# Optimization experiments

Measured on AMD Instinct MI355X. Metric: run time of the kernel, lower is better.

Reference implementation:

```python
import jax, jax.numpy as jnp
import numpy as np
import math

B, S, D = 2, 2048, 1024
H, KV, HD = 16, 4, 64
N_REP = H // KV
ROPE_THETA = 1.0e6


def _rope_tables(seq_len, head_dim, theta):
    inv_freq = 1.0 / (theta ** (np.arange(0, head_dim, 2, dtype=np.float32) / head_dim))
    t = np.arange(seq_len, dtype=np.float32)
    freqs = np.outer(t, inv_freq)                      # [S, HD/2]
    emb = np.concatenate([freqs, freqs], axis=-1)      # [S, HD]
    return jnp.asarray(np.cos(emb)), jnp.asarray(np.sin(emb))


def setup_inputs() -> dict:
    key = jax.random.key(0)
    ks = jax.random.split(key, 6)
    cos, sin = _rope_tables(S, HD, ROPE_THETA)
    scale = 0.02
    return {
        "x": jax.random.normal(ks[0], (B, S, D), dtype=jnp.float32),
        "cos": cos,
        "sin": sin,
        "Wq": jax.random.normal(ks[1], (D, H * HD), dtype=jnp.float32) * scale,
        "Wk": jax.random.normal(ks[2], (D, KV * HD), dtype=jnp.float32) * scale,
        "Wv": jax.random.normal(ks[3], (D, KV * HD), dtype=jnp.float32) * scale,
        "Wo": jax.random.normal(ks[4], (H * HD, D), dtype=jnp.float32) * scale,
    }


def _rotate_half(u):
    u1, u2 = u[..., : HD // 2], u[..., HD // 2 :]
    return jnp.concatenate([-u2, u1], axis=-1)


def reference(x, cos, sin, Wq, Wk, Wv, Wo):
    bsz, seq_len, _ = x.shape
    q = (x @ Wq).reshape(bsz, seq_len, H, HD)   # [B,S,H,HD]
    k = (x @ Wk).reshape(bsz, seq_len, KV, HD)  # [B,S,KV,HD]
    v = (x @ Wv).reshape(bsz, seq_len, KV, HD)

    # RoPE: cos/sin [S,HD] broadcast over batch and heads (unsqueeze_dim=1)
    c = cos[:seq_len][None, :, None, :]
    s = sin[:seq_len][None, :, None, :]
    q = q * c + _rotate_half(q) * s
    k = k * c + _rotate_half(k) * s

    # repeat_kv: expand KV heads groupwise to H heads
    k = jnp.repeat(k, N_REP, axis=2)  # [B,S,H,HD]
    v = jnp.repeat(v, N_REP, axis=2)

    q = q.transpose(0, 2, 1, 3)  # [B,H,S,HD]
    k = k.transpose(0, 2, 1, 3)
    v = v.transpose(0, 2, 1, 3)

    scores = jnp.einsum("bhqd,bhkd->bhqk", q, k) / math.sqrt(HD)
    causal = jnp.tril(jnp.ones((seq_len, seq_len), dtype=bool))
    scores = jnp.where(causal[None, None], scores, jnp.finfo(jnp.float32).min)
    probs = jax.nn.softmax(scores.astype(jnp.float32), axis=-1).astype(x.dtype)

    out = jnp.einsum("bhqk,bhkd->bhqd", probs, v)        # [B,H,S,HD]
    out = out.transpose(0, 2, 1, 3).reshape(bsz, seq_len, H * HD)
    return out @ Wo
```

## Files before the change

kernel.cpp:

```cpp
#include <hip/hip_runtime.h>

#define SS 2048
#define NH 16
#define NKV 4
#define HD 64

typedef __bf16 bf16;
typedef __bf16 bf16x8 __attribute__((ext_vector_type(8)));
typedef float f32x4 __attribute__((ext_vector_type(4)));

#define SM_SCALE 0.18033688011f

__device__ __forceinline__ void gl_lds16(const bf16* g, bf16* l) {
    __builtin_amdgcn_global_load_lds((const __attribute__((address_space(1))) void*)g,
                                     (__attribute__((address_space(3))) void*)l, 16, 0, 0);
}

__global__ __launch_bounds__(256) void prep_kernel(
    const float* __restrict__ x, const float* __restrict__ Wq, const float* __restrict__ Wk,
    const float* __restrict__ Wv, const float* __restrict__ Wo,
    bf16* __restrict__ xb, bf16* __restrict__ wqkv_t, bf16* __restrict__ wo_t)
{
    const int blk = blockIdx.x;
    const int tid = threadIdx.x;
    if (blk >= 640) {
        const float4* xv = (const float4*)x;
        const size_t base = (size_t)(blk - 640) * 2048 + tid;
        #pragma unroll
        for (int j = 0; j < 8; ++j) {
            const float4 v = xv[base + j * 256];
            bf16* o = xb + (base + j * 256) * 4;
            o[0] = (bf16)v.x; o[1] = (bf16)v.y; o[2] = (bf16)v.z; o[3] = (bf16)v.w;
        }
        return;
    }
    const float* W; bf16* Wt; int N, n0, k0;
    if (blk < 256)      { W = Wq; Wt = wqkv_t;                       N = 1024; n0 = (blk & 15) * 64;         k0 = (blk >> 4) * 64; }
    else if (blk < 320) { W = Wk; Wt = wqkv_t + (size_t)1024 * 1024; N = 256;  n0 = ((blk - 256) & 3) * 64;  k0 = ((blk - 256) >> 2) * 64; }
    else if (blk < 384) { W = Wv; Wt = wqkv_t + (size_t)1280 * 1024; N = 256;  n0 = ((blk - 320) & 3) * 64;  k0 = ((blk - 320) >> 2) * 64; }
    else                { W = Wo; Wt = wo_t;                         N = 1024; n0 = ((blk - 384) & 15) * 64; k0 = ((blk - 384) >> 4) * 64; }

    __shared__ float Ts[64][65];
    const int c = tid & 63, rr = tid >> 6;
    #pragma unroll
    for (int i = 0; i < 16; ++i) {
        const int kk = i * 4 + rr;
        Ts[kk][c] = W[(size_t)(k0 + kk) * N + n0 + c];
    }
    __syncthreads();
    #pragma unroll
    for (int i = 0; i < 16; ++i) {
        const int nn = i * 4 + rr;
        Wt[(size_t)(n0 + nn) * 1024 + k0 + c] = (bf16)Ts[c][nn];
    }
}

template<int EPI>
__global__ __launch_bounds__(256) void gemm_bt_kernel(
    const bf16* __restrict__ A, const bf16* __restrict__ Bt, float* __restrict__ C,
    const float* __restrict__ cosp, const float* __restrict__ sinp,
    bf16* __restrict__ qo, bf16* __restrict__ ko, bf16* __restrict__ vto,
    int M, int N, int K)
{
    __shared__ bf16 As[64 * 32];
    __shared__ bf16 Bs[128 * 32];
    const int m0 = blockIdx.x * 64, n0 = blockIdx.y * 128;
    const int tid = threadIdx.x;
    const int w = tid >> 6, lane = tid & 63, g = lane >> 4, li = lane & 15;
    const int wm = w >> 1, wn = w & 1;

    f32x4 acc[2][4];
    const f32x4 z = {0.f, 0.f, 0.f, 0.f};
    #pragma unroll
    for (int i = 0; i < 2; ++i)
        #pragma unroll
        for (int j = 0; j < 4; ++j) acc[i][j] = z;

    const int srow = tid >> 2, schunk = (tid & 3) * 8;
    const bf16* pA  = A  + (size_t)(m0 + srow) * K + schunk;
    const bf16* pB0 = Bt + (size_t)(n0 + srow) * K + schunk;
    const bf16* pB1 = Bt + (size_t)(n0 + 64 + srow) * K + schunk;
    bf16* lA  = As + (size_t)w * 512;
    bf16* lB0 = Bs + (size_t)w * 512;
    bf16* lB1 = Bs + 2048 + (size_t)w * 512;

    for (int kk = 0; kk < K; kk += 32) {
        __syncthreads();
        gl_lds16(pA + kk, lA);
        gl_lds16(pB0 + kk, lB0);
        gl_lds16(pB1 + kk, lB1);
        __syncthreads();
        bf16x8 af[2], bfr[4];
        #pragma unroll
        for (int mi = 0; mi < 2; ++mi) af[mi] = *(const bf16x8*)&As[(wm * 32 + mi * 16 + li) * 32 + g * 8];
        #pragma unroll
        for (int ni = 0; ni < 4; ++ni) bfr[ni] = *(const bf16x8*)&Bs[(wn * 64 + ni * 16 + li) * 32 + g * 8];
        #pragma unroll
        for (int mi = 0; mi < 2; ++mi)
            #pragma unroll
            for (int ni = 0; ni < 4; ++ni)
                acc[mi][ni] = __builtin_amdgcn_mfma_f32_16x16x32_bf16(af[mi], bfr[ni], acc[mi][ni], 0, 0, 0);
    }

    const int row0 = m0 + wm * 32, col0 = n0 + wn * 64;
    if (EPI == 0) {
        #pragma unroll
        for (int mi = 0; mi < 2; ++mi)
            #pragma unroll
            for (int ni = 0; ni < 4; ++ni)
                #pragma unroll
                for (int r = 0; r < 4; ++r)
                    C[(size_t)(row0 + mi * 16 + g * 4 + r) * N + col0 + ni * 16 + li] = acc[mi][ni][r];
    } else {
        #pragma unroll
        for (int ni = 0; ni < 4; ++ni) {
            const int col = col0 + ni * 16 + li;
            const int d = col & 63;
            #pragma unroll
            for (int mi = 0; mi < 2; ++mi) {
                #pragma unroll
                for (int r = 0; r < 4; ++r) {
                    const int row = row0 + mi * 16 + g * 4 + r;
                    const int bb = row >> 11, s = row & 2047;
                    float val = acc[mi][ni][r];
                    if (col < 1280) {
                        const float pairv = acc[mi][ni ^ 2][r];
                        const float rot = (d < 32) ? -pairv : pairv;
                        val = val * cosp[s * 64 + d] + rot * sinp[s * 64 + d];
                    }
                    if (col < 1024) {
                        const int hh = col >> 6;
                        qo[(((size_t)bb * NH + hh) * SS + s) * HD + d] = (bf16)(val * SM_SCALE);
                    } else if (col < 1280) {
                        const int kh = (col - 1024) >> 6;
                        ko[(((size_t)bb * NKV + kh) * SS + s) * HD + d] = (bf16)val;
                    } else {
                        const int kh = (col - 1280) >> 6;
                        vto[(((size_t)bb * NKV + kh) * HD + d) * SS + s] = (bf16)val;
                    }
                }
            }
        }
    }
}

#define FP 72
#define FPV 136
__global__ __launch_bounds__(256) void flash_kernel(const bf16* __restrict__ q, const bf16* __restrict__ k,
                                                    const bf16* __restrict__ vt, bf16* __restrict__ o)
{
    __shared__ bf16 Ks[128][FP];
    __shared__ bf16 Vt[64][FPV];
    __shared__ bf16 Ps[4][16][FP];

    const int blk = blockIdx.x;
    const int qt = 31 - (blk >> 5);
    const int h = blk & 15;
    const int b = (blk >> 4) & 1;
    const int kvh = h >> 2;
    const int tid = threadIdx.x;
    const int w = tid >> 6, lane = tid & 63, g = lane >> 4, li = lane & 15;

    const bf16* qh = q + ((size_t)b * NH + h) * SS * HD;
    const bf16* kh = k + ((size_t)b * NKV + kvh) * SS * HD;
    const bf16* vh = vt + ((size_t)b * NKV + kvh) * (size_t)HD * SS;

    bf16x8 ones;
    #pragma unroll
    for (int j = 0; j < 8; ++j) ones[j] = (bf16)1.0f;
    const f32x4 z = {0.f, 0.f, 0.f, 0.f};

    const bf16* qrow = qh + (size_t)(qt * 64 + w * 16 + li) * HD;
    bf16x8 qf[2];
    qf[0] = *(const bf16x8*)(qrow + g * 8);
    qf[1] = *(const bf16x8*)(qrow + 32 + g * 8);

    f32x4 o_acc[4], l_acc;
    #pragma unroll
    for (int nt = 0; nt < 4; ++nt) o_acc[nt] = z;
    l_acc = z;

    for (int kt0 = 0; kt0 <= qt; kt0 += 2) {
        __syncthreads();
        {
            const int krow = tid >> 1, kcol = (tid & 1) * 32;
            const uint4* ks = (const uint4*)(kh + (size_t)(kt0 * 64 + krow) * HD + kcol);
            const uint4 a0 = ks[0], a1 = ks[1], a2 = ks[2], a3 = ks[3];
            *(uint4*)&Ks[krow][kcol]      = a0;
            *(uint4*)&Ks[krow][kcol + 8]  = a1;
            *(uint4*)&Ks[krow][kcol + 16] = a2;
            *(uint4*)&Ks[krow][kcol + 24] = a3;
            const int vrow = tid >> 2, vcol = (tid & 3) * 32;
            const uint4* vs = (const uint4*)(vh + (size_t)vrow * SS + kt0 * 64 + vcol);
            const uint4 c0 = vs[0], c1 = vs[1], c2 = vs[2], c3 = vs[3];
            *(uint4*)&Vt[vrow][vcol]      = c0;
            *(uint4*)&Vt[vrow][vcol + 8]  = c1;
            *(uint4*)&Vt[vrow][vcol + 16] = c2;
            *(uint4*)&Vt[vrow][vcol + 24] = c3;
        }
        __syncthreads();

        #pragma unroll
        for (int sub = 0; sub < 2; ++sub) {
            const int kt = kt0 + sub;
            if (kt > qt) break;

            f32x4 s_acc[4];
            #pragma unroll
            for (int nt = 0; nt < 4; ++nt) s_acc[nt] = z;
            #pragma unroll
            for (int t = 0; t < 2; ++t)
                #pragma unroll
                for (int nt = 0; nt < 4; ++nt) {
                    const bf16x8 kf = *(const bf16x8*)&Ks[sub * 64 + nt * 16 + li][t * 32 + g * 8];
                    s_acc[nt] = __builtin_amdgcn_mfma_f32_16x16x32_bf16(qf[t], kf, s_acc[nt], 0, 0, 0);
                }

            if (kt == qt) {
                const int qr0 = qt * 64 + w * 16 + g * 4;
                #pragma unroll
                for (int nt = 0; nt < 4; ++nt) {
                    const int key = kt * 64 + nt * 16 + li;
                    #pragma unroll
                    for (int r = 0; r < 4; ++r) {
                        float sv = s_acc[nt][r];
                        if (key > qr0 + r) sv = -1e30f;
                        Ps[w][g * 4 + r][(nt * 16 + li) ^ (g * 16)] = (bf16)exp2f(sv);
                    }
                }
            } else {
                #pragma unroll
                for (int nt = 0; nt < 4; ++nt)
                    #pragma unroll
                    for (int r = 0; r < 4; ++r)
                        Ps[w][g * 4 + r][(nt * 16 + li) ^ (g * 16)] = (bf16)exp2f(s_acc[nt][r]);
            }

            #pragma unroll
            for (int t = 0; t < 2; ++t) {
                const bf16x8 pf = *(const bf16x8*)&Ps[w][li][(t * 32 + g * 8) ^ ((li >> 2) * 16)];
                l_acc = __builtin_amdgcn_mfma_f32_16x16x32_bf16(pf, ones, l_acc, 0, 0, 0);
                #pragma unroll
                for (int nt = 0; nt < 4; ++nt) {
                    const bf16x8 vf = *(const bf16x8*)&Vt[nt * 16 + li][sub * 64 + t * 32 + g * 8];
                    o_acc[nt] = __builtin_amdgcn_mfma_f32_16x16x32_bf16(pf, vf, o_acc[nt], 0, 0, 0);
                }
            }
        }
    }

    #pragma unroll
    for (int r = 0; r < 4; ++r) {
        const float inv = 1.f / l_acc[r];
        const int s = qt * 64 + w * 16 + g * 4 + r;
        bf16* orow = o + (((size_t)b * SS + s) * NH + h) * HD;
        #pragma unroll
        for (int nt = 0; nt < 4; ++nt) orow[nt * 16 + li] = (bf16)(o_acc[nt][r] * inv);
    }
}

extern "C" void kernel_launch(void* const* d_in, const int* in_sizes, int n_in,
                              void* d_out, int out_size, void* d_ws, size_t ws_size,
                              hipStream_t stream) {
    const float* x     = (const float*)d_in[0];
    const float* cos_t = (const float*)d_in[1];
    const float* sin_t = (const float*)d_in[2];
    const float* Wq    = (const float*)d_in[3];
    const float* Wk    = (const float*)d_in[4];
    const float* Wv    = (const float*)d_in[5];
    const float* Wo    = (const float*)d_in[6];
    float* out = (float*)d_out;

    char* wsb = (char*)d_ws;
    bf16* x_b    = (bf16*)(wsb);
    bf16* wqkv_t = (bf16*)(wsb + 8388608);
    bf16* wo_t   = (bf16*)(wsb + 11534336);
    bf16* q_b    = (bf16*)(wsb + 13631488);
    bf16* k_b    = (bf16*)(wsb + 22020096);
    bf16* vt_b   = (bf16*)(wsb + 24117248);
    bf16* o_b    = x_b;

    prep_kernel<<<1152, 256, 0, stream>>>(x, Wq, Wk, Wv, Wo, x_b, wqkv_t, wo_t);

    gemm_bt_kernel<2><<<dim3(64, 12), 256, 0, stream>>>(x_b, wqkv_t, nullptr, cos_t, sin_t,
                                                        q_b, k_b, vt_b, 4096, 1536, 1024);
    flash_kernel<<<1024, 256, 0, stream>>>(q_b, k_b, vt_b, o_b);
    gemm_bt_kernel<0><<<dim3(64, 8), 256, 0, stream>>>(o_b, wo_t, out, nullptr, nullptr,
                                                       nullptr, nullptr, nullptr, 4096, 1024, 1024);
}
```

Before: 182.1 us.

## Fuse x bf16 cast into QKV GEMM, widen K-tile, swizzle LDS with async loads

```diff
diff --git a/kernel.cpp b/kernel.cpp
--- a/kernel.cpp
+++ b/kernel.cpp
@@ -17,23 +17,12 @@
 }
 
 __global__ __launch_bounds__(256) void prep_kernel(
-    const float* __restrict__ x, const float* __restrict__ Wq, const float* __restrict__ Wk,
+    const float* __restrict__ Wq, const float* __restrict__ Wk,
     const float* __restrict__ Wv, const float* __restrict__ Wo,
-    bf16* __restrict__ xb, bf16* __restrict__ wqkv_t, bf16* __restrict__ wo_t)
+    bf16* __restrict__ wqkv_t, bf16* __restrict__ wo_t)
 {
     const int blk = blockIdx.x;
     const int tid = threadIdx.x;
-    if (blk >= 640) {
-        const float4* xv = (const float4*)x;
-        const size_t base = (size_t)(blk - 640) * 2048 + tid;
-        #pragma unroll
-        for (int j = 0; j < 8; ++j) {
-            const float4 v = xv[base + j * 256];
-            bf16* o = xb + (base + j * 256) * 4;
-            o[0] = (bf16)v.x; o[1] = (bf16)v.y; o[2] = (bf16)v.z; o[3] = (bf16)v.w;
-        }
-        return;
-    }
     const float* W; bf16* Wt; int N, n0, k0;
     if (blk < 256)      { W = Wq; Wt = wqkv_t;                       N = 1024; n0 = (blk & 15) * 64;         k0 = (blk >> 4) * 64; }
     else if (blk < 320) { W = Wk; Wt = wqkv_t + (size_t)1024 * 1024; N = 256;  n0 = ((blk - 256) & 3) * 64;  k0 = ((blk - 256) >> 2) * 64; }
@@ -57,13 +46,14 @@
 
 template<int EPI>
 __global__ __launch_bounds__(256) void gemm_bt_kernel(
-    const bf16* __restrict__ A, const bf16* __restrict__ Bt, float* __restrict__ C,
+    const bf16* __restrict__ A, const float* __restrict__ Af,
+    const bf16* __restrict__ Bt, float* __restrict__ C,
     const float* __restrict__ cosp, const float* __restrict__ sinp,
     bf16* __restrict__ qo, bf16* __restrict__ ko, bf16* __restrict__ vto,
     int M, int N, int K)
 {
-    __shared__ bf16 As[64 * 32];
-    __shared__ bf16 Bs[128 * 32];
+    __shared__ bf16 As[64 * 64];
+    __shared__ bf16 Bs[128 * 64];
     const int m0 = blockIdx.x * 64, n0 = blockIdx.y * 128;
     const int tid = threadIdx.x;
     const int w = tid >> 6, lane = tid & 63, g = lane >> 4, li = lane & 15;
@@ -76,30 +66,57 @@
         #pragma unroll
         for (int j = 0; j < 4; ++j) acc[i][j] = z;
 
-    const int srow = tid >> 2, schunk = (tid & 3) * 8;
-    const bf16* pA  = A  + (size_t)(m0 + srow) * K + schunk;
+    const int srow = tid >> 3;
+    const int schunk = ((tid & 7) ^ (srow & 7)) * 8;
     const bf16* pB0 = Bt + (size_t)(n0 + srow) * K + schunk;
-    const bf16* pB1 = Bt + (size_t)(n0 + 64 + srow) * K + schunk;
-    bf16* lA  = As + (size_t)w * 512;
+    const bf16* pB1 = Bt + (size_t)(n0 + 32 + srow) * K + schunk;
+    const bf16* pB2 = Bt + (size_t)(n0 + 64 + srow) * K + schunk;
+    const bf16* pB3 = Bt + (size_t)(n0 + 96 + srow) * K + schunk;
     bf16* lB0 = Bs + (size_t)w * 512;
     bf16* lB1 = Bs + 2048 + (size_t)w * 512;
-
-    for (int kk = 0; kk < K; kk += 32) {
+    bf16* lB2 = Bs + 4096 + (size_t)w * 512;
+    bf16* lB3 = Bs + 6144 + (size_t)w * 512;
+    const bf16* pA0 = (EPI == 0) ? A + (size_t)(m0 + srow) * K + schunk : nullptr;
+    const bf16* pA1 = (EPI == 0) ? A + (size_t)(m0 + 32 + srow) * K + schunk : nullptr;
+    bf16* lA0 = As + (size_t)w * 512;
+    bf16* lA1 = As + 2048 + (size_t)w * 512;
+
+    for (int kk = 0; kk < K; kk += 64) {
         __syncthreads();
-        gl_lds16(pA + kk, lA);
+        if (EPI == 0) {
+            gl_lds16(pA0 + kk, lA0);
+            gl_lds16(pA1 + kk, lA1);
+        } else {
+            #pragma unroll
+            for (int s = 0; s < 2; ++s) {
+                const float* src = Af + (size_t)(m0 + s * 32 + srow) * K + kk + (tid & 7) * 8;
+                const float4 v0 = *(const float4*)src;
+                const float4 v1 = *(const float4*)(src + 4);
+                bf16x8 t8;
+                t8[0] = (bf16)v0.x; t8[1] = (bf16)v0.y; t8[2] = (bf16)v0.z; t8[3] = (bf16)v0.w;
+                t8[4] = (bf16)v1.x; t8[5] = (bf16)v1.y; t8[6] = (bf16)v1.z; t8[7] = (bf16)v1.w;
+                *(bf16x8*)&As[(s * 32 + srow) * 64 + schunk] = t8;
+            }
+        }
         gl_lds16(pB0 + kk, lB0);
         gl_lds16(pB1 + kk, lB1);
+        gl_lds16(pB2 + kk, lB2);
+        gl_lds16(pB3 + kk, lB3);
         __syncthreads();
-        bf16x8 af[2], bfr[4];
-        #pragma unroll
-        for (int mi = 0; mi < 2; ++mi) af[mi] = *(const bf16x8*)&As[(wm * 32 + mi * 16 + li) * 32 + g * 8];
-        #pragma unroll
-        for (int ni = 0; ni < 4; ++ni) bfr[ni] = *(const bf16x8*)&Bs[(wn * 64 + ni * 16 + li) * 32 + g * 8];
-        #pragma unroll
-        for (int mi = 0; mi < 2; ++mi)
-            #pragma unroll
-            for (int ni = 0; ni < 4; ++ni)
-                acc[mi][ni] = __builtin_amdgcn_mfma_f32_16x16x32_bf16(af[mi], bfr[ni], acc[mi][ni], 0, 0, 0);
+        #pragma unroll
+        for (int t = 0; t < 2; ++t) {
+            const int phys = ((t * 4 + g) ^ (li & 7)) * 8;
+            bf16x8 af[2], bfr[4];
+            #pragma unroll
+            for (int mi = 0; mi < 2; ++mi) af[mi] = *(const bf16x8*)&As[(wm * 32 + mi * 16 + li) * 64 + phys];
+            #pragma unroll
+            for (int ni = 0; ni < 4; ++ni) bfr[ni] = *(const bf16x8*)&Bs[(wn * 64 + ni * 16 + li) * 64 + phys];
+            #pragma unroll
+            for (int mi = 0; mi < 2; ++mi)
+                #pragma unroll
+                for (int ni = 0; ni < 4; ++ni)
+                    acc[mi][ni] = __builtin_amdgcn_mfma_f32_16x16x32_bf16(af[mi], bfr[ni], acc[mi][ni], 0, 0, 0);
+        }
     }
 
     const int row0 = m0 + wm * 32, col0 = n0 + wn * 64;
@@ -144,14 +161,12 @@
     }
 }
 
-#define FP 72
-#define FPV 136
 __global__ __launch_bounds__(256) void flash_kernel(const bf16* __restrict__ q, const bf16* __restrict__ k,
                                                     const bf16* __restrict__ vt, bf16* __restrict__ o)
 {
-    __shared__ bf16 Ks[128][FP];
-    __shared__ bf16 Vt[64][FPV];
-    __shared__ bf16 Ps[4][16][FP];
+    __shared__ bf16 Ks[128 * 64];
+    __shared__ bf16 Vt[64 * 128];
+    __shared__ bf16 Ps[4][16][72];
 
     const int blk = blockIdx.x;
     const int qt = 31 - (blk >> 5);
@@ -175,6 +190,13 @@
     qf[0] = *(const bf16x8*)(qrow + g * 8);
     qf[1] = *(const bf16x8*)(qrow + 32 + g * 8);
 
+    const int ksrow = tid >> 3;
+    const int kchunk = ((tid & 7) ^ (ksrow & 7)) * 8;
+    const int vsrow = tid >> 4;
+    const int vchunk = (((tid & 15) ^ (vsrow & 7)) & 15) * 8;
+    bf16* lK = Ks + (size_t)w * 512;
+    bf16* lV = Vt + (size_t)w * 512;
+
     f32x4 o_acc[4], l_acc;
     #pragma unroll
     for (int nt = 0; nt < 4; ++nt) o_acc[nt] = z;
@@ -183,20 +205,12 @@
     for (int kt0 = 0; kt0 <= qt; kt0 += 2) {
         __syncthreads();
         {
-            const int krow = tid >> 1, kcol = (tid & 1) * 32;
-            const uint4* ks = (const uint4*)(kh + (size_t)(kt0 * 64 + krow) * HD + kcol);
-            const uint4 a0 = ks[0], a1 = ks[1], a2 = ks[2], a3 = ks[3];
-            *(uint4*)&Ks[krow][kcol]      = a0;
-            *(uint4*)&Ks[krow][kcol + 8]  = a1;
-            *(uint4*)&Ks[krow][kcol + 16] = a2;
-            *(uint4*)&Ks[krow][kcol + 24] = a3;
-            const int vrow = tid >> 2, vcol = (tid & 3) * 32;
-            const uint4* vs = (const uint4*)(vh + (size_t)vrow * SS + kt0 * 64 + vcol);
-            const uint4 c0 = vs[0], c1 = vs[1], c2 = vs[2], c3 = vs[3];
-            *(uint4*)&Vt[vrow][vcol]      = c0;
-            *(uint4*)&Vt[vrow][vcol + 8]  = c1;
-            *(uint4*)&Vt[vrow][vcol + 16] = c2;
-            *(uint4*)&Vt[vrow][vcol + 24] = c3;
+            #pragma unroll
+            for (int s = 0; s < 4; ++s)
+                gl_lds16(kh + (size_t)(kt0 * 64 + s * 32 + ksrow) * HD + kchunk, lK + s * 2048);
+            #pragma unroll
+            for (int s = 0; s < 4; ++s)
+                gl_lds16(vh + (size_t)(s * 16 + vsrow) * SS + kt0 * 64 + vchunk, lV + s * 2048);
         }
         __syncthreads();
 
@@ -212,7 +226,7 @@
             for (int t = 0; t < 2; ++t)
                 #pragma unroll
                 for (int nt = 0; nt < 4; ++nt) {
-                    const bf16x8 kf = *(const bf16x8*)&Ks[sub * 64 + nt * 16 + li][t * 32 + g * 8];
+                    const bf16x8 kf = *(const bf16x8*)&Ks[(sub * 64 + nt * 16 + li) * 64 + (((t * 4 + g) ^ (li & 7)) * 8)];
                     s_acc[nt] = __builtin_amdgcn_mfma_f32_16x16x32_bf16(qf[t], kf, s_acc[nt], 0, 0, 0);
                 }
 
@@ -242,7 +256,7 @@
                 l_acc = __builtin_amdgcn_mfma_f32_16x16x32_bf16(pf, ones, l_acc, 0, 0, 0);
                 #pragma unroll
                 for (int nt = 0; nt < 4; ++nt) {
-                    const bf16x8 vf = *(const bf16x8*)&Vt[nt * 16 + li][sub * 64 + t * 32 + g * 8];
+                    const bf16x8 vf = *(const bf16x8*)&Vt[(nt * 16 + li) * 128 + (((sub * 8 + t * 4 + g) ^ (li & 7)) * 8)];
                     o_acc[nt] = __builtin_amdgcn_mfma_f32_16x16x32_bf16(pf, vf, o_acc[nt], 0, 0, 0);
                 }
             }
@@ -272,19 +286,18 @@
     float* out = (float*)d_out;
 
     char* wsb = (char*)d_ws;
-    bf16* x_b    = (bf16*)(wsb);
+    bf16* o_b    = (bf16*)(wsb);
     bf16* wqkv_t = (bf16*)(wsb + 8388608);
     bf16* wo_t   = (bf16*)(wsb + 11534336);
     bf16* q_b    = (bf16*)(wsb + 13631488);
     bf16* k_b    = (bf16*)(wsb + 22020096);
     bf16* vt_b   = (bf16*)(wsb + 24117248);
-    bf16* o_b    = x_b;
-
-    prep_kernel<<<1152, 256, 0, stream>>>(x, Wq, Wk, Wv, Wo, x_b, wqkv_t, wo_t);
-
-    gemm_bt_kernel<2><<<dim3(64, 12), 256, 0, stream>>>(x_b, wqkv_t, nullptr, cos_t, sin_t,
+
+    prep_kernel<<<640, 256, 0, stream>>>(Wq, Wk, Wv, Wo, wqkv_t, wo_t);
+
+    gemm_bt_kernel<2><<<dim3(64, 12), 256, 0, stream>>>(nullptr, x, wqkv_t, nullptr, cos_t, sin_t,
                                                         q_b, k_b, vt_b, 4096, 1536, 1024);
     flash_kernel<<<1024, 256, 0, stream>>>(q_b, k_b, vt_b, o_b);
-    gemm_bt_kernel<0><<<dim3(64, 8), 256, 0, stream>>>(o_b, wo_t, out, nullptr, nullptr,
+    gemm_bt_kernel<0><<<dim3(64, 8), 256, 0, stream>>>(o_b, nullptr, wo_t, out, nullptr, nullptr,
                                                        nullptr, nullptr, nullptr, 4096, 1024, 1024);
 }
```

After: 167.2 us. 1.09x faster.

## Use single-wave GEMM tiles with XCD mapping and swizzled async LDS loads in flash

Applied to the files above, without the earlier changes.

```diff
diff --git a/kernel.cpp b/kernel.cpp
--- a/kernel.cpp
+++ b/kernel.cpp
@@ -56,71 +56,76 @@
 }
 
 template<int EPI>
-__global__ __launch_bounds__(256) void gemm_bt_kernel(
+__global__ __launch_bounds__(64) void gemm1w_kernel(
     const bf16* __restrict__ A, const bf16* __restrict__ Bt, float* __restrict__ C,
     const float* __restrict__ cosp, const float* __restrict__ sinp,
     bf16* __restrict__ qo, bf16* __restrict__ ko, bf16* __restrict__ vto,
     int M, int N, int K)
 {
     __shared__ bf16 As[64 * 32];
-    __shared__ bf16 Bs[128 * 32];
-    const int m0 = blockIdx.x * 64, n0 = blockIdx.y * 128;
-    const int tid = threadIdx.x;
-    const int w = tid >> 6, lane = tid & 63, g = lane >> 4, li = lane & 15;
-    const int wm = w >> 1, wn = w & 1;
-
-    f32x4 acc[2][4];
+    __shared__ bf16 Bs[64 * 32];
+    const int nbc = N >> 6;
+    const int xcd = blockIdx.x & 7, kidx = blockIdx.x >> 3;
+    const int mb = xcd * 8 + kidx / nbc, nb = kidx % nbc;
+    const int m0 = mb * 64, n0 = nb * 64;
+    const int lane = threadIdx.x;
+    const int g = lane >> 4, li = lane & 15;
+
+    f32x4 acc[4][4];
     const f32x4 z = {0.f, 0.f, 0.f, 0.f};
     #pragma unroll
-    for (int i = 0; i < 2; ++i)
+    for (int i = 0; i < 4; ++i)
         #pragma unroll
         for (int j = 0; j < 4; ++j) acc[i][j] = z;
 
-    const int srow = tid >> 2, schunk = (tid & 3) * 8;
-    const bf16* pA  = A  + (size_t)(m0 + srow) * K + schunk;
-    const bf16* pB0 = Bt + (size_t)(n0 + srow) * K + schunk;
-    const bf16* pB1 = Bt + (size_t)(n0 + 64 + srow) * K + schunk;
-    bf16* lA  = As + (size_t)w * 512;
-    bf16* lB0 = Bs + (size_t)w * 512;
-    bf16* lB1 = Bs + 2048 + (size_t)w * 512;
+    const int srow = lane >> 2;
+    const int schunk = ((lane & 3) ^ ((lane >> 3) & 3)) * 8;
+    const bf16* pA[4]; const bf16* pB[4];
+    #pragma unroll
+    for (int s = 0; s < 4; ++s) {
+        pA[s] = A + (size_t)(m0 + s * 16 + srow) * K + schunk;
+        pB[s] = Bt + (size_t)(n0 + s * 16 + srow) * K + schunk;
+    }
 
     for (int kk = 0; kk < K; kk += 32) {
         __syncthreads();
-        gl_lds16(pA + kk, lA);
-        gl_lds16(pB0 + kk, lB0);
-        gl_lds16(pB1 + kk, lB1);
-        __syncthreads();
-        bf16x8 af[2], bfr[4];
-        #pragma unroll
-        for (int mi = 0; mi < 2; ++mi) af[mi] = *(const bf16x8*)&As[(wm * 32 + mi * 16 + li) * 32 + g * 8];
-        #pragma unroll
-        for (int ni = 0; ni < 4; ++ni) bfr[ni] = *(const bf16x8*)&Bs[(wn * 64 + ni * 16 + li) * 32 + g * 8];
-        #pragma unroll
-        for (int mi = 0; mi < 2; ++mi)
+        #pragma unroll
+        for (int s = 0; s < 4; ++s) gl_lds16(pA[s] + kk, As + s * 512);
+        #pragma unroll
+        for (int s = 0; s < 4; ++s) gl_lds16(pB[s] + kk, Bs + s * 512);
+        __syncthreads();
+
+        const int phys = ((g ^ ((li >> 1) & 3)) * 8);
+        bf16x8 af[4], bfr[4];
+        #pragma unroll
+        for (int mi = 0; mi < 4; ++mi) af[mi] = *(const bf16x8*)&As[(mi * 16 + li) * 32 + phys];
+        #pragma unroll
+        for (int ni = 0; ni < 4; ++ni) bfr[ni] = *(const bf16x8*)&Bs[(ni * 16 + li) * 32 + phys];
+        #pragma unroll
+        for (int mi = 0; mi < 4; ++mi)
             #pragma unroll
             for (int ni = 0; ni < 4; ++ni)
                 acc[mi][ni] = __builtin_amdgcn_mfma_f32_16x16x32_bf16(af[mi], bfr[ni], acc[mi][ni], 0, 0, 0);
     }
 
-    const int row0 = m0 + wm * 32, col0 = n0 + wn * 64;
     if (EPI == 0) {
         #pragma unroll
-        for (int mi = 0; mi < 2; ++mi)
+        for (int mi = 0; mi < 4; ++mi)
             #pragma unroll
             for (int ni = 0; ni < 4; ++ni)
                 #pragma unroll
                 for (int r = 0; r < 4; ++r)
-                    C[(size_t)(row0 + mi * 16 + g * 4 + r) * N + col0 + ni * 16 + li] = acc[mi][ni][r];
+                    C[(size_t)(m0 + mi * 16 + g * 4 + r) * N + n0 + ni * 16 + li] = acc[mi][ni][r];
     } else {
         #pragma unroll
         for (int ni = 0; ni < 4; ++ni) {
-            const int col = col0 + ni * 16 + li;
+            const int col = n0 + ni * 16 + li;
             const int d = col & 63;
             #pragma unroll
-            for (int mi = 0; mi < 2; ++mi) {
+            for (int mi = 0; mi < 4; ++mi) {
                 #pragma unroll
                 for (int r = 0; r < 4; ++r) {
-                    const int row = row0 + mi * 16 + g * 4 + r;
+                    const int row = m0 + mi * 16 + g * 4 + r;
                     const int bb = row >> 11, s = row & 2047;
                     float val = acc[mi][ni][r];
                     if (col < 1280) {
@@ -144,14 +149,12 @@
     }
 }
 
-#define FP 72
-#define FPV 136
 __global__ __launch_bounds__(256) void flash_kernel(const bf16* __restrict__ q, const bf16* __restrict__ k,
                                                     const bf16* __restrict__ vt, bf16* __restrict__ o)
 {
-    __shared__ bf16 Ks[128][FP];
-    __shared__ bf16 Vt[64][FPV];
-    __shared__ bf16 Ps[4][16][FP];
+    __shared__ bf16 Ks[128 * 64];
+    __shared__ bf16 Vt[64 * 128];
+    __shared__ bf16 Ps[4][16][64];
 
     const int blk = blockIdx.x;
     const int qt = 31 - (blk >> 5);
@@ -175,6 +178,13 @@
     qf[0] = *(const bf16x8*)(qrow + g * 8);
     qf[1] = *(const bf16x8*)(qrow + 32 + g * 8);
 
+    const int ksrow = tid >> 3;
+    const int kchunk = ((tid & 7) ^ (ksrow & 7)) * 8;
+    const int vsrow = tid >> 4;
+    const int vchunk = (((tid & 15) ^ (vsrow & 7)) & 15) * 8;
+    bf16* lK = Ks + (size_t)w * 512;
+    bf16* lV = Vt + (size_t)w * 512;
+
     f32x4 o_acc[4], l_acc;
     #pragma unroll
     for (int nt = 0; nt < 4; ++nt) o_acc[nt] = z;
@@ -183,20 +193,12 @@
     for (int kt0 = 0; kt0 <= qt; kt0 += 2) {
         __syncthreads();
         {
-            const int krow = tid >> 1, kcol = (tid & 1) * 32;
-            const uint4* ks = (const uint4*)(kh + (size_t)(kt0 * 64 + krow) * HD + kcol);
-            const uint4 a0 = ks[0], a1 = ks[1], a2 = ks[2], a3 = ks[3];
-            *(uint4*)&Ks[krow][kcol]      = a0;
-            *(uint4*)&Ks[krow][kcol + 8]  = a1;
-            *(uint4*)&Ks[krow][kcol + 16] = a2;
-            *(uint4*)&Ks[krow][kcol + 24] = a3;
-            const int vrow = tid >> 2, vcol = (tid & 3) * 32;
-            const uint4* vs = (const uint4*)(vh + (size_t)vrow * SS + kt0 * 64 + vcol);
-            const uint4 c0 = vs[0], c1 = vs[1], c2 = vs[2], c3 = vs[3];
-            *(uint4*)&Vt[vrow][vcol]      = c0;
-            *(uint4*)&Vt[vrow][vcol + 8]  = c1;
-            *(uint4*)&Vt[vrow][vcol + 16] = c2;
-            *(uint4*)&Vt[vrow][vcol + 24] = c3;
+            #pragma unroll
+            for (int s = 0; s < 4; ++s)
+                gl_lds16(kh + (size_t)(kt0 * 64 + s * 32 + ksrow) * HD + kchunk, lK + s * 2048);
+            #pragma unroll
+            for (int s = 0; s < 4; ++s)
+                gl_lds16(vh + (size_t)(s * 16 + vsrow) * SS + kt0 * 64 + vchunk, lV + s * 2048);
         }
         __syncthreads();
 
@@ -212,7 +214,7 @@
             for (int t = 0; t < 2; ++t)
                 #pragma unroll
                 for (int nt = 0; nt < 4; ++nt) {
-                    const bf16x8 kf = *(const bf16x8*)&Ks[sub * 64 + nt * 16 + li][t * 32 + g * 8];
+                    const bf16x8 kf = *(const bf16x8*)&Ks[(sub * 64 + nt * 16 + li) * 64 + (((t * 4 + g) ^ (li & 7)) * 8)];
                     s_acc[nt] = __builtin_amdgcn_mfma_f32_16x16x32_bf16(qf[t], kf, s_acc[nt], 0, 0, 0);
                 }
 
@@ -242,7 +244,7 @@
                 l_acc = __builtin_amdgcn_mfma_f32_16x16x32_bf16(pf, ones, l_acc, 0, 0, 0);
                 #pragma unroll
                 for (int nt = 0; nt < 4; ++nt) {
-                    const bf16x8 vf = *(const bf16x8*)&Vt[nt * 16 + li][sub * 64 + t * 32 + g * 8];
+                    const bf16x8 vf = *(const bf16x8*)&Vt[(nt * 16 + li) * 128 + (((sub * 8 + t * 4 + g) ^ (li & 7)) * 8)];
                     o_acc[nt] = __builtin_amdgcn_mfma_f32_16x16x32_bf16(pf, vf, o_acc[nt], 0, 0, 0);
                 }
             }
@@ -282,9 +284,9 @@
 
     prep_kernel<<<1152, 256, 0, stream>>>(x, Wq, Wk, Wv, Wo, x_b, wqkv_t, wo_t);
 
-    gemm_bt_kernel<2><<<dim3(64, 12), 256, 0, stream>>>(x_b, wqkv_t, nullptr, cos_t, sin_t,
-                                                        q_b, k_b, vt_b, 4096, 1536, 1024);
+    gemm1w_kernel<2><<<1536, 64, 0, stream>>>(x_b, wqkv_t, nullptr, cos_t, sin_t,
+                                              q_b, k_b, vt_b, 4096, 1536, 1024);
     flash_kernel<<<1024, 256, 0, stream>>>(q_b, k_b, vt_b, o_b);
-    gemm_bt_kernel<0><<<dim3(64, 8), 256, 0, stream>>>(o_b, wo_t, out, nullptr, nullptr,
-                                                       nullptr, nullptr, nullptr, 4096, 1024, 1024);
-}
+    gemm1w_kernel<0><<<1024, 64, 0, stream>>>(o_b, wo_t, out, nullptr, nullptr,
+                                              nullptr, nullptr, nullptr, 4096, 1024, 1024);
+}
```

Measured after the change: 190.6 us. 1.05x slower.
